# Performance work log

Measured on AMD Instinct MI355X. Metric: run time of the kernel, lower is better.

Reference implementation:

```python
import jax, jax.numpy as jnp
import numpy as np

MOMENTUM = 0.01


def setup_inputs() -> dict:
    key = jax.random.key(0)
    k1, k2, k3 = jax.random.split(key, 3)
    B, C, D = 4096, 100000, 256
    inputs = jax.random.normal(k1, (B, D), dtype=jnp.float32)
    targets = jax.random.randint(k2, (B,), 0, C, dtype=jnp.int64)
    features_memory = jax.random.normal(k3, (C, D), dtype=jnp.float32)
    return {"inputs": inputs, "targets": targets, "features_memory": features_memory}


def reference(inputs, targets, features_memory):
    # Sequential per-sample momentum update + L2 row-normalize, honoring
    # index collisions exactly as the original Python loop does.
    def step(feat, xy):
        x, y = xy
        row = feat[y]  # [D]
        new = MOMENTUM * row + (1.0 - MOMENTUM) * x
        new = new / jnp.linalg.norm(new)
        return feat.at[y].set(new), None

    feat, _ = jax.lax.scan(step, features_memory, (inputs, targets))
    return feat
```

## Files before the change

kernel.cpp:

```cpp
#include <hip/hip_runtime.h>
#include <hip/hip_bf16.h>

#define NB 4096
#define NC 100000
#define ND 256
#define MOM 0.01f

typedef float f32x4 __attribute__((ext_vector_type(4)));

__global__ __launch_bounds__(256) void mb_copy_kernel(
        const f32x4* __restrict__ src, f32x4* __restrict__ dst) {
    int base = blockIdx.x * 2048 + threadIdx.x;
    f32x4 v0 = src[base];
    f32x4 v1 = src[base + 256];
    f32x4 v2 = src[base + 512];
    f32x4 v3 = src[base + 768];
    f32x4 v4 = src[base + 1024];
    f32x4 v5 = src[base + 1280];
    f32x4 v6 = src[base + 1536];
    f32x4 v7 = src[base + 1792];
    __builtin_nontemporal_store(v0, dst + base);
    __builtin_nontemporal_store(v1, dst + base + 256);
    __builtin_nontemporal_store(v2, dst + base + 512);
    __builtin_nontemporal_store(v3, dst + base + 768);
    __builtin_nontemporal_store(v4, dst + base + 1024);
    __builtin_nontemporal_store(v5, dst + base + 1280);
    __builtin_nontemporal_store(v6, dst + base + 1536);
    __builtin_nontemporal_store(v7, dst + base + 1792);
}

__global__ __launch_bounds__(256) void mb_chain_kernel(
        const float* __restrict__ inputs,
        const int* __restrict__ targets,
        const float* __restrict__ feat_in,
        float* __restrict__ out) {
    __shared__ int4 tg4[NB / 4];

    int t = threadIdx.x;
    #pragma unroll
    for (int k = 0; k < 4; ++k)
        tg4[t + k * 256] = reinterpret_cast<const int4*>(targets)[t + k * 256];
    __syncthreads();

    const int* tg = reinterpret_cast<const int*>(tg4);
    int wave = (blockIdx.x * 256 + t) >> 6;
    int lane = t & 63;
    int y = tg[wave];

    for (int base = 0; base < wave; base += 256) {
        int4 v = tg4[(base >> 2) + lane];
        int j0 = base + lane * 4;
        bool m = (j0 < wave && v.x == y) | (j0 + 1 < wave && v.y == y)
               | (j0 + 2 < wave && v.z == y) | (j0 + 3 < wave && v.w == y);
        if (__ballot(m)) return;
    }

    float4 row = *reinterpret_cast<const float4*>(
        feat_in + (size_t)y * ND + lane * 4);

    for (int base = wave & ~255; base < NB; base += 256) {
        int4 v = tg4[(base >> 2) + lane];
        int j0 = base + lane * 4;
        unsigned lm = 0;
        lm |= (j0     >= wave && v.x == y) ? 1u : 0u;
        lm |= (j0 + 1 >= wave && v.y == y) ? 2u : 0u;
        lm |= (j0 + 2 >= wave && v.z == y) ? 4u : 0u;
        lm |= (j0 + 3 >= wave && v.w == y) ? 8u : 0u;
        unsigned long long wm = __ballot(lm != 0);
        while (wm) {
            int L = __ffsll((long long)wm) - 1;
            wm &= wm - 1ull;
            unsigned lmL = (unsigned)__shfl((int)lm, L);
            while (lmL) {
                int k = __ffs((int)lmL) - 1;
                lmL &= lmL - 1u;
                int jj = base + L * 4 + k;
                float4 x = *reinterpret_cast<const float4*>(
                    inputs + (size_t)jj * ND + lane * 4);
                row.x = fmaf(MOM, row.x, (1.0f - MOM) * x.x);
                row.y = fmaf(MOM, row.y, (1.0f - MOM) * x.y);
                row.z = fmaf(MOM, row.z, (1.0f - MOM) * x.z);
                row.w = fmaf(MOM, row.w, (1.0f - MOM) * x.w);
                float ss = row.x * row.x + row.y * row.y
                         + row.z * row.z + row.w * row.w;
                #pragma unroll
                for (int off = 32; off > 0; off >>= 1)
                    ss += __shfl_xor(ss, off);
                float inv = 1.0f / sqrtf(ss);
                row.x *= inv; row.y *= inv; row.z *= inv; row.w *= inv;
            }
        }
    }

    *reinterpret_cast<float4*>(out + (size_t)y * ND + lane * 4) = row;
}

extern "C" void kernel_launch(void* const* d_in, const int* in_sizes, int n_in,
                              void* d_out, int out_size, void* d_ws, size_t ws_size,
                              hipStream_t stream) {
    const float* inputs  = (const float*)d_in[0];
    const int*   targets = (const int*)d_in[1];
    const float* feat    = (const float*)d_in[2];
    float* out = (float*)d_out;

    mb_copy_kernel<<<3125, 256, 0, stream>>>(
        (const f32x4*)feat, (f32x4*)out);

    mb_chain_kernel<<<NB / 4, 256, 0, stream>>>(inputs, targets, feat, out);
}
```

Before: 41.91 us.

## Fuse copy and chain kernels into one launch, skipping targeted rows in copy

Merges the bulk memory-bank copy and the per-target update chain into a single kernel, split by block index. Copy blocks scan all targets into a shared flag array and skip writing any row that a chain block will overwrite. This removes the ordering dependency and the second launch, so the copy and chain work can overlap. In exchange, every copy block reads the whole targets array, and the stores are no longer nontemporal.

Result: faster. 37.67 us (-10.1%).

```diff
diff --git a/kernel.cpp b/kernel.cpp
--- a/kernel.cpp
+++ b/kernel.cpp
@@ -6,93 +6,117 @@
 #define ND 256
 #define MOM 0.01f
 
+#define CHAIN_BLOCKS (NB / 4)
+#define COPY_BLOCKS  ((NC * ND / 4) / 2048)
+
 typedef float f32x4 __attribute__((ext_vector_type(4)));
 
-__global__ __launch_bounds__(256) void mb_copy_kernel(
-        const f32x4* __restrict__ src, f32x4* __restrict__ dst) {
-    int base = blockIdx.x * 2048 + threadIdx.x;
-    f32x4 v0 = src[base];
-    f32x4 v1 = src[base + 256];
-    f32x4 v2 = src[base + 512];
-    f32x4 v3 = src[base + 768];
-    f32x4 v4 = src[base + 1024];
-    f32x4 v5 = src[base + 1280];
-    f32x4 v6 = src[base + 1536];
-    f32x4 v7 = src[base + 1792];
-    __builtin_nontemporal_store(v0, dst + base);
-    __builtin_nontemporal_store(v1, dst + base + 256);
-    __builtin_nontemporal_store(v2, dst + base + 512);
-    __builtin_nontemporal_store(v3, dst + base + 768);
-    __builtin_nontemporal_store(v4, dst + base + 1024);
-    __builtin_nontemporal_store(v5, dst + base + 1280);
-    __builtin_nontemporal_store(v6, dst + base + 1536);
-    __builtin_nontemporal_store(v7, dst + base + 1792);
-}
-
-__global__ __launch_bounds__(256) void mb_chain_kernel(
+__global__ __launch_bounds__(256) void mb_fused_kernel(
         const float* __restrict__ inputs,
         const int* __restrict__ targets,
         const float* __restrict__ feat_in,
         float* __restrict__ out) {
     __shared__ int4 tg4[NB / 4];
+    __shared__ int flags[32];
+    int t = threadIdx.x;
 
-    int t = threadIdx.x;
-    #pragma unroll
-    for (int k = 0; k < 4; ++k)
-        tg4[t + k * 256] = reinterpret_cast<const int4*>(targets)[t + k * 256];
-    __syncthreads();
+    if (blockIdx.x < CHAIN_BLOCKS) {
+        #pragma unroll
+        for (int k = 0; k < 4; ++k)
+            tg4[t + k * 256] =
+                reinterpret_cast<const int4*>(targets)[t + k * 256];
+        __syncthreads();
 
-    const int* tg = reinterpret_cast<const int*>(tg4);
-    int wave = (blockIdx.x * 256 + t) >> 6;
-    int lane = t & 63;
-    int y = tg[wave];
+        const int* tg = reinterpret_cast<const int*>(tg4);
+        int wave = (blockIdx.x * 256 + t) >> 6;
+        int lane = t & 63;
+        int y = tg[wave];
 
-    for (int base = 0; base < wave; base += 256) {
-        int4 v = tg4[(base >> 2) + lane];
-        int j0 = base + lane * 4;
-        bool m = (j0 < wave && v.x == y) | (j0 + 1 < wave && v.y == y)
-               | (j0 + 2 < wave && v.z == y) | (j0 + 3 < wave && v.w == y);
-        if (__ballot(m)) return;
-    }
+        for (int base = 0; base < wave; base += 256) {
+            int4 v = tg4[(base >> 2) + lane];
+            int j0 = base + lane * 4;
+            bool m = (j0 < wave && v.x == y) | (j0 + 1 < wave && v.y == y)
+                   | (j0 + 2 < wave && v.z == y) | (j0 + 3 < wave && v.w == y);
+            if (__ballot(m)) return;
+        }
 
-    float4 row = *reinterpret_cast<const float4*>(
-        feat_in + (size_t)y * ND + lane * 4);
+        float4 row = *reinterpret_cast<const float4*>(
+            feat_in + (size_t)y * ND + lane * 4);
 
-    for (int base = wave & ~255; base < NB; base += 256) {
-        int4 v = tg4[(base >> 2) + lane];
-        int j0 = base + lane * 4;
-        unsigned lm = 0;
-        lm |= (j0     >= wave && v.x == y) ? 1u : 0u;
-        lm |= (j0 + 1 >= wave && v.y == y) ? 2u : 0u;
-        lm |= (j0 + 2 >= wave && v.z == y) ? 4u : 0u;
-        lm |= (j0 + 3 >= wave && v.w == y) ? 8u : 0u;
-        unsigned long long wm = __ballot(lm != 0);
-        while (wm) {
-            int L = __ffsll((long long)wm) - 1;
-            wm &= wm - 1ull;
-            unsigned lmL = (unsigned)__shfl((int)lm, L);
-            while (lmL) {
-                int k = __ffs((int)lmL) - 1;
-                lmL &= lmL - 1u;
-                int jj = base + L * 4 + k;
-                float4 x = *reinterpret_cast<const float4*>(
-                    inputs + (size_t)jj * ND + lane * 4);
-                row.x = fmaf(MOM, row.x, (1.0f - MOM) * x.x);
-                row.y = fmaf(MOM, row.y, (1.0f - MOM) * x.y);
-                row.z = fmaf(MOM, row.z, (1.0f - MOM) * x.z);
-                row.w = fmaf(MOM, row.w, (1.0f - MOM) * x.w);
-                float ss = row.x * row.x + row.y * row.y
-                         + row.z * row.z + row.w * row.w;
-                #pragma unroll
-                for (int off = 32; off > 0; off >>= 1)
-                    ss += __shfl_xor(ss, off);
-                float inv = 1.0f / sqrtf(ss);
-                row.x *= inv; row.y *= inv; row.z *= inv; row.w *= inv;
+        for (int base = wave & ~255; base < NB; base += 256) {
+            int4 v = tg4[(base >> 2) + lane];
+            int j0 = base + lane * 4;
+            unsigned lm = 0;
+            lm |= (j0     >= wave && v.x == y) ? 1u : 0u;
+            lm |= (j0 + 1 >= wave && v.y == y) ? 2u : 0u;
+            lm |= (j0 + 2 >= wave && v.z == y) ? 4u : 0u;
+            lm |= (j0 + 3 >= wave && v.w == y) ? 8u : 0u;
+            unsigned long long wm = __ballot(lm != 0);
+            while (wm) {
+                int L = __ffsll((long long)wm) - 1;
+                wm &= wm - 1ull;
+                unsigned lmL = (unsigned)__shfl((int)lm, L);
+                while (lmL) {
+                    int k = __ffs((int)lmL) - 1;
+                    lmL &= lmL - 1u;
+                    int jj = base + L * 4 + k;
+                    float4 x = *reinterpret_cast<const float4*>(
+                        inputs + (size_t)jj * ND + lane * 4);
+                    row.x = fmaf(MOM, row.x, (1.0f - MOM) * x.x);
+                    row.y = fmaf(MOM, row.y, (1.0f - MOM) * x.y);
+                    row.z = fmaf(MOM, row.z, (1.0f - MOM) * x.z);
+                    row.w = fmaf(MOM, row.w, (1.0f - MOM) * x.w);
+                    float ss = row.x * row.x + row.y * row.y
+                             + row.z * row.z + row.w * row.w;
+                    #pragma unroll
+                    for (int off = 32; off > 0; off >>= 1)
+                        ss += __shfl_xor(ss, off);
+                    float inv = 1.0f / sqrtf(ss);
+                    row.x *= inv; row.y *= inv; row.z *= inv; row.w *= inv;
+                }
             }
         }
+
+        *reinterpret_cast<float4*>(out + (size_t)y * ND + lane * 4) = row;
+    } else {
+        int cb = blockIdx.x - CHAIN_BLOCKS;
+        int r0 = cb * 32;
+
+        if (t < 32) flags[t] = 0;
+        __syncthreads();
+
+        const int4* tgg = reinterpret_cast<const int4*>(targets);
+        #pragma unroll
+        for (int k = 0; k < 4; ++k) {
+            int4 v = tgg[t + k * 256];
+            if ((unsigned)(v.x - r0) < 32u) flags[v.x - r0] = 1;
+            if ((unsigned)(v.y - r0) < 32u) flags[v.y - r0] = 1;
+            if ((unsigned)(v.z - r0) < 32u) flags[v.z - r0] = 1;
+            if ((unsigned)(v.w - r0) < 32u) flags[v.w - r0] = 1;
+        }
+        __syncthreads();
+
+        const f32x4* src = reinterpret_cast<const f32x4*>(feat_in);
+        f32x4* dst = reinterpret_cast<f32x4*>(out);
+        size_t base = (size_t)cb * 2048 + t;
+        f32x4 v0 = src[base];
+        f32x4 v1 = src[base + 256];
+        f32x4 v2 = src[base + 512];
+        f32x4 v3 = src[base + 768];
+        f32x4 v4 = src[base + 1024];
+        f32x4 v5 = src[base + 1280];
+        f32x4 v6 = src[base + 1536];
+        f32x4 v7 = src[base + 1792];
+        int w = t >> 6;
+        if (!flags[w     ]) dst[base]        = v0;
+        if (!flags[w +  4]) dst[base +  256] = v1;
+        if (!flags[w +  8]) dst[base +  512] = v2;
+        if (!flags[w + 12]) dst[base +  768] = v3;
+        if (!flags[w + 16]) dst[base + 1024] = v4;
+        if (!flags[w + 20]) dst[base + 1280] = v5;
+        if (!flags[w + 24]) dst[base + 1536] = v6;
+        if (!flags[w + 28]) dst[base + 1792] = v7;
     }
-
-    *reinterpret_cast<float4*>(out + (size_t)y * ND + lane * 4) = row;
 }
 
 extern "C" void kernel_launch(void* const* d_in, const int* in_sizes, int n_in,
@@ -103,8 +127,6 @@
     const float* feat    = (const float*)d_in[2];
     float* out = (float*)d_out;
 
-    mb_copy_kernel<<<3125, 256, 0, stream>>>(
-        (const f32x4*)feat, (f32x4*)out);
-
-    mb_chain_kernel<<<NB / 4, 256, 0, stream>>>(inputs, targets, feat, out);
+    mb_fused_kernel<<<CHAIN_BLOCKS + COPY_BLOCKS, 256, 0, stream>>>(
+        inputs, targets, feat, out);
 }
```
